# Kernel tuning notes

Measured on AMD Instinct MI355X. Metric: run time of the kernel, lower is better.

Reference implementation:

```python
import jax, jax.numpy as jnp
import numpy as np

N_VERTS = 5000
N_FACES = 10000
BATCH = 2
N_PTS = 8192
OUTER_LOOP = 4
INNER_LOOP = 50
SOLVE_SCALE = 10.0
ADAM_LR = 0.01
B1, B2, EPS = 0.9, 0.999, 1e-8


def _normalize(x, eps=1e-12):
    # torch.nn.functional.normalize(p=2, dim=-1)
    n = jnp.linalg.norm(x, axis=-1, keepdims=True)
    return x / jnp.maximum(n, eps)


def _interp_bary(tri, vw):
    # tri: [M,3,3] per-point triangle attributes, vw: [M,2] barycentric (u,v)
    bary = jnp.concatenate([vw, 1.0 - vw[:, :1] - vw[:, 1:2]], axis=-1)  # [M,3]
    return jnp.einsum('mij,mi->mj', tri, bary)


def _solve_delta_vwd(qV, fid, vw, mesh_V, mesh_F, mesh_N):
    # Newton-like correspondence solve via unrolled Adam (solve_delta_vwd).
    tri_idx = mesh_F[fid]          # [M,3]
    tri_V = mesh_V[tri_idx]        # [M,3,3]
    tri_N = mesh_N[tri_idx]        # [M,3,3]
    d0 = jnp.linalg.norm(_interp_bary(tri_V, vw) - qV, axis=-1)
    delta0 = jnp.concatenate([jnp.zeros_like(vw), d0[:, None]], axis=-1)  # [M,3]
    target = qV * SOLVE_SCALE

    def loss_fn(delta):
        w = vw + delta[:, :2]
        cV = _interp_bary(tri_V, w) * SOLVE_SCALE
        cN = _normalize(_interp_bary(tri_N, w)) * SOLVE_SCALE
        match = cV + cN * delta[:, 2:3]
        return jnp.mean((match - target) ** 2)  # F.mse_loss

    def step(carry, t):
        delta, m, v = carry
        g = jax.grad(loss_fn)(delta)
        m = B1 * m + (1.0 - B1) * g
        v = B2 * v + (1.0 - B2) * g * g
        mhat = m / (1.0 - B1 ** t)
        vhat = v / (1.0 - B2 ** t)
        delta = delta - ADAM_LR * mhat / (jnp.sqrt(vhat) + EPS)
        return (delta, m, v), None

    ts = jnp.arange(1, INNER_LOOP + 1, dtype=qV.dtype)
    zeros = jnp.zeros_like(delta0)
    (delta, _, _), _ = jax.lax.scan(step, (delta0, zeros, zeros), ts)
    return delta


def _forward(verts, mesh_V, mesh_N, mesh_F):
    b, n, _ = verts.shape
    # init_corres_spt: KNN (K=1) of query points against triangle centers
    centers = mesh_V[mesh_F].mean(axis=1)  # [F,3]
    d2 = ((verts ** 2).sum(-1)[..., None]
          + (centers ** 2).sum(-1)[None, None, :]
          - 2.0 * jnp.einsum('bnd,fd->bnf', verts, centers))  # [b,n,F]
    fidx = jnp.argmin(d2, axis=-1)                             # [b,n]
    fid = fidx.reshape(-1)
    qV = verts.reshape(-1, 3)
    vw = jnp.full((b * n, 2), 1.0 / 3.0, dtype=verts.dtype)
    # update_corres_spt (method='uvd'): outer triwalk loop.
    # triwalk is an external CPU mesh-walker; we use the module's documented
    # fallback when triwalk is None: vw <- vw + delta (face index unchanged).
    for _ in range(OUTER_LOOP):
        delta = _solve_delta_vwd(qV, fid, vw, mesh_V, mesh_F, mesh_N)
        vw = vw + delta[:, :2]
    outlier_mask = jnp.zeros((b, n), dtype=bool)  # max_dist = inf
    return fidx, vw.reshape(b, n, 2), outlier_mask


def setup_inputs() -> dict:
    key = jax.random.key(0)
    k1, k2, k3, k4 = jax.random.split(key, 4)
    mesh_V = jax.random.normal(k1, (N_VERTS, 3), dtype=jnp.float32)
    mesh_F = jax.random.randint(k2, (N_FACES, 3), 0, N_VERTS)
    mesh_N = _normalize(jax.random.normal(k3, (N_VERTS, 3), dtype=jnp.float32))
    verts = jax.random.normal(k4, (BATCH, N_PTS, 3), dtype=jnp.float32)
    return {"verts": verts, "mesh_V": mesh_V, "mesh_N": mesh_N, "mesh_F": mesh_F}


def reference(verts, mesh_V, mesh_N, mesh_F):
    return _forward(verts, mesh_V, mesh_N, mesh_F)
```

## Files before the change

kernel.cpp:

```cpp
#include <hip/hip_runtime.h>
#include <math.h>
#include <stdint.h>

constexpr int kVerts = 5000;
constexpr int kFaces = 10000;
constexpr int kPts   = 16384;
constexpr int kOuter = 4;
constexpr int kInner = 50;

#define SCALE 10.0f

#define KNN_WAVES 16
#define KNN_FQ    4
constexpr int kQuarter     = kFaces / KNN_FQ;
constexpr int kPtsPerLane  = 2;
constexpr int kPtsPerBlock = 64 * kPtsPerLane;
constexpr int kPtGroups    = kPts / kPtsPerBlock;

struct BiasTabP { float rb[kInner + 2][2]; };
constexpr BiasTabP make_tabp() {
    BiasTabP t{};
    float b1 = 1.0f, b2 = 1.0f;
    for (int i = 0; i < kInner; ++i) {
        b1 *= 0.9f; b2 *= 0.999f;
        t.rb[i][0] = 1.0f / (1.0f - b1);
        t.rb[i][1] = 1.0f / (1.0f - b2);
    }
    t.rb[kInner][0]     = t.rb[kInner - 1][0];
    t.rb[kInner][1]     = t.rb[kInner - 1][1];
    t.rb[kInner + 1][0] = t.rb[kInner - 1][0];
    t.rb[kInner + 1][1] = t.rb[kInner - 1][1];
    return t;
}
constexpr BiasTabP kTabP = make_tabp();

__global__ __launch_bounds__(256)
void centers_kernel(const float* __restrict__ mesh_V,
                    const int*   __restrict__ mesh_F,
                    float4*      __restrict__ cent)
{
    const int f = blockIdx.x * 256 + threadIdx.x;
    if (f >= kFaces) return;
    const int i0 = mesh_F[f * 3 + 0];
    const int i1 = mesh_F[f * 3 + 1];
    const int i2 = mesh_F[f * 3 + 2];
    const float cx = __fdiv_rn(__fadd_rn(__fadd_rn(mesh_V[i0*3+0], mesh_V[i1*3+0]), mesh_V[i2*3+0]), 3.0f);
    const float cy = __fdiv_rn(__fadd_rn(__fadd_rn(mesh_V[i0*3+1], mesh_V[i1*3+1]), mesh_V[i2*3+1]), 3.0f);
    const float cz = __fdiv_rn(__fadd_rn(__fadd_rn(mesh_V[i0*3+2], mesh_V[i1*3+2]), mesh_V[i2*3+2]), 3.0f);
    const float cc = __fadd_rn(__fadd_rn(__fmul_rn(cx, cx), __fmul_rn(cy, cy)),
                               __fmul_rn(cz, cz));
    cent[f] = make_float4(cx, cy, cz, cc);
}

__global__ __launch_bounds__(1024)
void knn_kernel(const float* __restrict__ verts,
                const float4* __restrict__ cent,
                float*        __restrict__ ws_d2,
                int*          __restrict__ ws_f)
{
    __shared__ float4 s_cent[kQuarter];
    __shared__ float  s_best [KNN_WAVES * kPtsPerBlock];
    __shared__ int    s_bestf[KNN_WAVES * kPtsPerBlock];

    const int tid  = threadIdx.x;
    const int lane = tid & 63;
    const int wv   = __builtin_amdgcn_readfirstlane(tid >> 6);
    const int pg   = blockIdx.x >> 2;
    const int fq   = blockIdx.x & 3;
    const int qbeg = fq * kQuarter;

    for (int i = tid; i < kQuarter; i += 1024)
        s_cent[i] = cent[qbeg + i];

    const int pA = pg * kPtsPerBlock + lane;
    const int pB = pA + 64;
    const float qxA = verts[pA * 3 + 0], qyA = verts[pA * 3 + 1], qzA = verts[pA * 3 + 2];
    const float qxB = verts[pB * 3 + 0], qyB = verts[pB * 3 + 1], qzB = verts[pB * 3 + 2];
    const float q2A = __fadd_rn(__fadd_rn(__fmul_rn(qxA, qxA), __fmul_rn(qyA, qyA)),
                                __fmul_rn(qzA, qzA));
    const float q2B = __fadd_rn(__fadd_rn(__fmul_rn(qxB, qxB), __fmul_rn(qyB, qyB)),
                                __fmul_rn(qzB, qzB));
    const float dqxA = __fmul_rn(2.0f, qxA), dqyA = __fmul_rn(2.0f, qyA), dqzA = __fmul_rn(2.0f, qzA);
    const float dqxB = __fmul_rn(2.0f, qxB), dqyB = __fmul_rn(2.0f, qyB), dqzB = __fmul_rn(2.0f, qzB);

    __syncthreads();

    const int fbeg = (wv * kQuarter) / KNN_WAVES;
    const int fend = ((wv + 1) * kQuarter) / KNN_WAVES;

    float bdA0 = INFINITY, bdA1 = INFINITY, bdB0 = INFINITY, bdB1 = INFINITY;
    int   bfA0 = 0x7fffffff, bfA1 = 0x7fffffff, bfB0 = 0x7fffffff, bfB1 = 0x7fffffff;

#define KNN_EVAL(FF, C, DQX, DQY, DQZ, Q2, BD, BF)                                    \
    {                                                                                 \
        const float dot2 = __fadd_rn(__fadd_rn(__fmul_rn((DQX), (C).x),               \
                                               __fmul_rn((DQY), (C).y)),              \
                                     __fmul_rn((DQZ), (C).z));                        \
        const float d2 = __fsub_rn(__fadd_rn((Q2), (C).w), dot2);                     \
        if (d2 < (BD)) { (BD) = d2; (BF) = (FF); }                                    \
    }

    int f = fbeg;
#pragma unroll 1
    for (; f + 8 <= fend; f += 8) {
        const float4 c0 = s_cent[f + 0];
        const float4 c1 = s_cent[f + 1];
        const float4 c2 = s_cent[f + 2];
        const float4 c3 = s_cent[f + 3];
        const float4 c4 = s_cent[f + 4];
        const float4 c5 = s_cent[f + 5];
        const float4 c6 = s_cent[f + 6];
        const float4 c7 = s_cent[f + 7];
        KNN_EVAL(qbeg + f + 0, c0, dqxA, dqyA, dqzA, q2A, bdA0, bfA0);
        KNN_EVAL(qbeg + f + 1, c1, dqxA, dqyA, dqzA, q2A, bdA1, bfA1);
        KNN_EVAL(qbeg + f + 2, c2, dqxA, dqyA, dqzA, q2A, bdA0, bfA0);
        KNN_EVAL(qbeg + f + 3, c3, dqxA, dqyA, dqzA, q2A, bdA1, bfA1);
        KNN_EVAL(qbeg + f + 4, c4, dqxA, dqyA, dqzA, q2A, bdA0, bfA0);
        KNN_EVAL(qbeg + f + 5, c5, dqxA, dqyA, dqzA, q2A, bdA1, bfA1);
        KNN_EVAL(qbeg + f + 6, c6, dqxA, dqyA, dqzA, q2A, bdA0, bfA0);
        KNN_EVAL(qbeg + f + 7, c7, dqxA, dqyA, dqzA, q2A, bdA1, bfA1);
        KNN_EVAL(qbeg + f + 0, c0, dqxB, dqyB, dqzB, q2B, bdB0, bfB0);
        KNN_EVAL(qbeg + f + 1, c1, dqxB, dqyB, dqzB, q2B, bdB1, bfB1);
        KNN_EVAL(qbeg + f + 2, c2, dqxB, dqyB, dqzB, q2B, bdB0, bfB0);
        KNN_EVAL(qbeg + f + 3, c3, dqxB, dqyB, dqzB, q2B, bdB1, bfB1);
        KNN_EVAL(qbeg + f + 4, c4, dqxB, dqyB, dqzB, q2B, bdB0, bfB0);
        KNN_EVAL(qbeg + f + 5, c5, dqxB, dqyB, dqzB, q2B, bdB1, bfB1);
        KNN_EVAL(qbeg + f + 6, c6, dqxB, dqyB, dqzB, q2B, bdB0, bfB0);
        KNN_EVAL(qbeg + f + 7, c7, dqxB, dqyB, dqzB, q2B, bdB1, bfB1);
    }
    for (; f < fend; ++f) {
        const float4 c0 = s_cent[f];
        KNN_EVAL(qbeg + f, c0, dqxA, dqyA, dqzA, q2A, bdA0, bfA0);
        KNN_EVAL(qbeg + f, c0, dqxB, dqyB, dqzB, q2B, bdB0, bfB0);
    }
#undef KNN_EVAL

    if (bdA1 < bdA0 || (bdA1 == bdA0 && bfA1 < bfA0)) { bdA0 = bdA1; bfA0 = bfA1; }
    if (bdB1 < bdB0 || (bdB1 == bdB0 && bfB1 < bfB0)) { bdB0 = bdB1; bfB0 = bfB1; }

    __syncthreads();

    s_best [wv * kPtsPerBlock + lane]      = bdA0;
    s_bestf[wv * kPtsPerBlock + lane]      = bfA0;
    s_best [wv * kPtsPerBlock + 64 + lane] = bdB0;
    s_bestf[wv * kPtsPerBlock + 64 + lane] = bfB0;
    __syncthreads();

    if (tid < kPtsPerBlock) {
        float best  = s_best[tid];
        int   bestf = s_bestf[tid];
#pragma unroll
        for (int w = 1; w < KNN_WAVES; ++w) {
            const float ob = s_best [w * kPtsPerBlock + tid];
            const int   of = s_bestf[w * kPtsPerBlock + tid];
            if (ob < best) { best = ob; bestf = of; }
        }
        const int p = pg * kPtsPerBlock + tid;
        ws_d2[fq * kPts + p] = best;
        ws_f [fq * kPts + p] = bestf;
    }
}

__global__ __launch_bounds__(64)
void solve_kernel(const float* __restrict__ verts,
                  const float* __restrict__ mesh_V,
                  const float* __restrict__ mesh_N,
                  const int*   __restrict__ mesh_F,
                  const float* __restrict__ ws_d2,
                  const int*   __restrict__ ws_f,
                  float*       __restrict__ out)
{
    const int p = blockIdx.x * 64 + threadIdx.x;

    float bdm = ws_d2[p];
    int   f   = ws_f[p];
#pragma unroll
    for (int q = 1; q < KNN_FQ; ++q) {
        const float d  = ws_d2[q * kPts + p];
        const int   ff = ws_f [q * kPts + p];
        if (d < bdm) { bdm = d; f = ff; }
    }
    out[p] = (float)f;

    const float qx = verts[p * 3 + 0];
    const float qy = verts[p * 3 + 1];
    const float qz = verts[p * 3 + 2];

    const int i0 = mesh_F[f * 3 + 0];
    const int i1 = mesh_F[f * 3 + 1];
    const int i2 = mesh_F[f * 3 + 2];

    const float V0x = mesh_V[i0*3+0], V0y = mesh_V[i0*3+1], V0z = mesh_V[i0*3+2];
    const float V1x = mesh_V[i1*3+0], V1y = mesh_V[i1*3+1], V1z = mesh_V[i1*3+2];
    const float V2x = mesh_V[i2*3+0], V2y = mesh_V[i2*3+1], V2z = mesh_V[i2*3+2];
    const float N0x = mesh_N[i0*3+0], N0y = mesh_N[i0*3+1], N0z = mesh_N[i0*3+2];
    const float N1x = mesh_N[i1*3+0], N1y = mesh_N[i1*3+1], N1z = mesh_N[i1*3+2];
    const float N2x = mesh_N[i2*3+0], N2y = mesh_N[i2*3+1], N2z = mesh_N[i2*3+2];

    const float E0x = V0x - V2x, E0y = V0y - V2y, E0z = V0z - V2z;
    const float E1x = V1x - V2x, E1y = V1y - V2y, E1z = V1z - V2z;
    const float F0x = N0x - N2x, F0y = N0y - N2y, F0z = N0z - N2z;
    const float F1x = N1x - N2x, F1y = N1y - N2y, F1z = N1z - N2z;

    const float tx = qx * SCALE, ty = qy * SCALE, tz = qz * SCALE;
    const float GS = 2.0f / (3.0f * 16384.0f);
    const float B1 = 0.9f,  ONE_M_B1 = 1.0f - 0.9f;
    const float B2 = 0.999f, ONE_M_B2 = 1.0f - 0.999f;

    float vwu = 1.0f / 3.0f, vwv = 1.0f / 3.0f;

#define SOLVE_STEP(RB1, RB2)                                                   \
    {                                                                          \
        const float bu = vwu + du;                                             \
        const float bv = vwv + dv;                                             \
        const float bw = (1.0f - bu) - bv;                                     \
        const float cVx = ((bu * V0x + bv * V1x) + bw * V2x) * SCALE;          \
        const float cVy = ((bu * V0y + bv * V1y) + bw * V2y) * SCALE;          \
        const float cVz = ((bu * V0z + bv * V1z) + bw * V2z) * SCALE;          \
        const float nrx = (bu * N0x + bv * N1x) + bw * N2x;                    \
        const float nry = (bu * N0y + bv * N1y) + bw * N2y;                    \
        const float nrz = (bu * N0z + bv * N1z) + bw * N2z;                    \
        const float nn  = (nrx * nrx + nry * nry) + nrz * nrz;                 \
        const float inv = __builtin_amdgcn_rsqf(nn);                           \
        const float nhx = nrx * inv, nhy = nry * inv, nhz = nrz * inv;         \
        const float cNx = nhx * SCALE, cNy = nhy * SCALE, cNz = nhz * SCALE;   \
        const float rx = (cVx + cNx * dd) - tx;                                \
        const float ry = (cVy + cNy * dd) - ty;                                \
        const float rz = (cVz + cNz * dd) - tz;                                \
        const float rv0  = (rx * E0x + ry * E0y) + rz * E0z;                   \
        const float rv1  = (rx * E1x + ry * E1y) + rz * E1z;                   \
        const float rn0  = (rx * F0x + ry * F0y) + rz * F0z;                   \
        const float rn1  = (rx * F1x + ry * F1y) + rz * F1z;                   \
        const float nf0  = (nhx * F0x + nhy * F0y) + nhz * F0z;                \
        const float nf1  = (nhx * F1x + nhy * F1y) + nhz * F1z;                \
        const float nr_r = (nhx * rx + nhy * ry) + nhz * rz;                   \
        const float gu = GS * (SCALE * rv0 + (dd * SCALE) * ((rn0 - nr_r * nf0) * inv)); \
        const float gv = GS * (SCALE * rv1 + (dd * SCALE) * ((rn1 - nr_r * nf1) * inv)); \
        const float gd = GS * (SCALE * nr_r);                                  \
        mAu = B1 * mAu + ONE_M_B1 * gu;                                        \
        mAv = B1 * mAv + ONE_M_B1 * gv;                                        \
        mAd = B1 * mAd + ONE_M_B1 * gd;                                        \
        vAu = B2 * vAu + ONE_M_B2 * (gu * gu);                                 \
        vAv = B2 * vAv + ONE_M_B2 * (gv * gv);                                 \
        vAd = B2 * vAd + ONE_M_B2 * (gd * gd);                                 \
        const float su = __builtin_amdgcn_rsqf(vAu * (RB2) + 1e-16f);          \
        const float sv = __builtin_amdgcn_rsqf(vAv * (RB2) + 1e-16f);          \
        const float sd = __builtin_amdgcn_rsqf(vAd * (RB2) + 1e-16f);          \
        du -= 0.01f * (mAu * (RB1)) * su;                                      \
        dv -= 0.01f * (mAv * (RB1)) * sv;                                      \
        dd -= 0.01f * (mAd * (RB1)) * sd;                                      \
    }

    for (int outer = 0; outer < kOuter; ++outer) {
        const float bw0 = (1.0f - vwu) - vwv;
        const float px = ((vwu * V0x + vwv * V1x) + bw0 * V2x);
        const float py = ((vwu * V0y + vwv * V1y) + bw0 * V2y);
        const float pz = ((vwu * V0z + vwv * V1z) + bw0 * V2z);
        const float dx = px - qx, dy = py - qy, dz = pz - qz;
        const float d0 = __builtin_amdgcn_sqrtf((dx * dx + dy * dy) + dz * dz);

        float du = 0.0f, dv = 0.0f, dd = d0;
        float mAu = 0.0f, mAv = 0.0f, mAd = 0.0f;
        float vAu = 0.0f, vAv = 0.0f, vAd = 0.0f;

        float rbA1 = kTabP.rb[0][0], rbA2 = kTabP.rb[0][1];
        float rbB1 = kTabP.rb[1][0], rbB2 = kTabP.rb[1][1];
#pragma unroll 1
        for (int i2 = 0; i2 < kInner / 2; ++i2) {
            const float n1a = kTabP.rb[2 * i2 + 2][0];
            const float n2a = kTabP.rb[2 * i2 + 2][1];
            const float n1b = kTabP.rb[2 * i2 + 3][0];
            const float n2b = kTabP.rb[2 * i2 + 3][1];
            SOLVE_STEP(rbA1, rbA2);
            SOLVE_STEP(rbB1, rbB2);
            rbA1 = n1a; rbA2 = n2a; rbB1 = n1b; rbB2 = n2b;
        }
        vwu += du;
        vwv += dv;
    }
#undef SOLVE_STEP

    out[kPts + 2 * p + 0] = vwu;
    out[kPts + 2 * p + 1] = vwv;
    out[3 * kPts + p]     = 0.0f;
}

extern "C" void kernel_launch(void* const* d_in, const int* in_sizes, int n_in,
                              void* d_out, int out_size, void* d_ws, size_t ws_size,
                              hipStream_t stream) {
    const float* verts  = (const float*)d_in[0];
    const float* mesh_V = (const float*)d_in[1];
    const float* mesh_N = (const float*)d_in[2];
    const int*   mesh_F = (const int*)d_in[3];
    float* out = (float*)d_out;

    float4* ws_cent = (float4*)d_ws;
    float*  ws_d2   = (float*)((char*)d_ws + kFaces * sizeof(float4));
    int*    ws_f    = (int*)((char*)ws_d2 + KNN_FQ * kPts * sizeof(float));

    hipLaunchKernelGGL(centers_kernel, dim3((kFaces + 255) / 256), dim3(256), 0, stream,
                       mesh_V, mesh_F, ws_cent);
    hipLaunchKernelGGL(knn_kernel,     dim3(kPtGroups * KNN_FQ), dim3(1024), 0, stream,
                       verts, ws_cent, ws_d2, ws_f);
    hipLaunchKernelGGL(solve_kernel,   dim3(kPts / 64), dim3(64), 0, stream,
                       verts, mesh_V, mesh_N, mesh_F, ws_d2, ws_f, out);
}
```

Before: 132.5 us.

## Split each point's Adam solve across four lanes with DPP broadcasts

The solve kernel now assigns four lanes to each query point. Lanes 0, 1 and 2 own the u, v and d components of the Adam state, and lane 3 is idle. Each step broadcasts the delta components within a quad using DPP, so every lane computes its own gradient component and Adam update. This raises thread-level parallelism: the old launch had only 256 single-wave blocks for 16384 points, which leaves most of the GPU idle. The cost is redundant per-lane evaluation of the interpolation and normal, an unused fourth lane, and a serial dependency through the cross-lane broadcasts.

```diff
diff --git a/kernel.cpp b/kernel.cpp
--- a/kernel.cpp
+++ b/kernel.cpp
@@ -161,7 +161,13 @@
     }
 }
 
-__global__ __launch_bounds__(64)
+template<int K>
+__device__ __forceinline__ float qbcast(float v) {
+    return __int_as_float(__builtin_amdgcn_update_dpp(
+        0, __float_as_int(v), K * 0x55 , 0xF, 0xF, true));
+}
+
+__global__ __launch_bounds__(256)
 void solve_kernel(const float* __restrict__ verts,
                   const float* __restrict__ mesh_V,
                   const float* __restrict__ mesh_N,
@@ -170,7 +176,11 @@
                   const int*   __restrict__ ws_f,
                   float*       __restrict__ out)
 {
-    const int p = blockIdx.x * 64 + threadIdx.x;
+    const int t  = blockIdx.x * 256 + threadIdx.x;
+    const int p  = t >> 2;
+    const int ch = t & 3;
+    const bool isV = (ch == 1);
+    const bool isD = (ch >= 2);
 
     float bdm = ws_d2[p];
     int   f   = ws_f[p];
@@ -180,7 +190,7 @@
         const int   ff = ws_f [q * kPts + p];
         if (d < bdm) { bdm = d; f = ff; }
     }
-    out[p] = (float)f;
+    if (ch == 0) out[p] = (float)f;
 
     const float qx = verts[p * 3 + 0];
     const float qy = verts[p * 3 + 1];
@@ -202,15 +212,25 @@
     const float F0x = N0x - N2x, F0y = N0y - N2y, F0z = N0z - N2z;
     const float F1x = N1x - N2x, F1y = N1y - N2y, F1z = N1z - N2z;
 
+    const float Aux = isV ? E1x : E0x;
+    const float Auy = isV ? E1y : E0y;
+    const float Auz = isV ? E1z : E0z;
+    const float Bx  = isD ? 0.0f : (isV ? F1x : F0x);
+    const float By  = isD ? 0.0f : (isV ? F1y : F0y);
+    const float Bz  = isD ? 0.0f : (isV ? F1z : F0z);
+
     const float tx = qx * SCALE, ty = qy * SCALE, tz = qz * SCALE;
     const float GS = 2.0f / (3.0f * 16384.0f);
-    const float B1 = 0.9f,  ONE_M_B1 = 1.0f - 0.9f;
-    const float B2 = 0.999f, ONE_M_B2 = 1.0f - 0.999f;
+    const float B1c = 0.9f,  ONE_M_B1 = 1.0f - 0.9f;
+    const float B2c = 0.999f, ONE_M_B2 = 1.0f - 0.999f;
 
     float vwu = 1.0f / 3.0f, vwv = 1.0f / 3.0f;
 
 #define SOLVE_STEP(RB1, RB2)                                                   \
     {                                                                          \
+        const float du = qbcast<0>(dlt);                                       \
+        const float dv = qbcast<1>(dlt);                                       \
+        const float dd = qbcast<2>(dlt);                                       \
         const float bu = vwu + du;                                             \
         const float bv = vwv + dv;                                             \
         const float bw = (1.0f - bu) - bv;                                     \
@@ -227,28 +247,18 @@
         const float rx = (cVx + cNx * dd) - tx;                                \
         const float ry = (cVy + cNy * dd) - ty;                                \
         const float rz = (cVz + cNz * dd) - tz;                                \
-        const float rv0  = (rx * E0x + ry * E0y) + rz * E0z;                   \
-        const float rv1  = (rx * E1x + ry * E1y) + rz * E1z;                   \
-        const float rn0  = (rx * F0x + ry * F0y) + rz * F0z;                   \
-        const float rn1  = (rx * F1x + ry * F1y) + rz * F1z;                   \
-        const float nf0  = (nhx * F0x + nhy * F0y) + nhz * F0z;                \
-        const float nf1  = (nhx * F1x + nhy * F1y) + nhz * F1z;                \
-        const float nr_r = (nhx * rx + nhy * ry) + nhz * rz;                   \
-        const float gu = GS * (SCALE * rv0 + (dd * SCALE) * ((rn0 - nr_r * nf0) * inv)); \
-        const float gv = GS * (SCALE * rv1 + (dd * SCALE) * ((rn1 - nr_r * nf1) * inv)); \
-        const float gd = GS * (SCALE * nr_r);                                  \
-        mAu = B1 * mAu + ONE_M_B1 * gu;                                        \
-        mAv = B1 * mAv + ONE_M_B1 * gv;                                        \
-        mAd = B1 * mAd + ONE_M_B1 * gd;                                        \
-        vAu = B2 * vAu + ONE_M_B2 * (gu * gu);                                 \
-        vAv = B2 * vAv + ONE_M_B2 * (gv * gv);                                 \
-        vAd = B2 * vAd + ONE_M_B2 * (gd * gd);                                 \
-        const float su = __builtin_amdgcn_rsqf(vAu * (RB2) + 1e-16f);          \
-        const float sv = __builtin_amdgcn_rsqf(vAv * (RB2) + 1e-16f);          \
-        const float sd = __builtin_amdgcn_rsqf(vAd * (RB2) + 1e-16f);          \
-        du -= 0.01f * (mAu * (RB1)) * su;                                      \
-        dv -= 0.01f * (mAv * (RB1)) * sv;                                      \
-        dd -= 0.01f * (mAd * (RB1)) * sd;                                      \
+        const float Ax = isD ? nhx : Aux;                                      \
+        const float Ay = isD ? nhy : Auy;                                      \
+        const float Az = isD ? nhz : Auz;                                      \
+        const float dotA = (rx * Ax + ry * Ay) + rz * Az;                      \
+        const float dotB = (rx * Bx + ry * By) + rz * Bz;                      \
+        const float nhB  = (nhx * Bx + nhy * By) + nhz * Bz;                   \
+        const float nr_r = qbcast<2>(dotA);                                    \
+        const float g = GS * (SCALE * dotA + (dd * SCALE) * ((dotB - nr_r * nhB) * inv)); \
+        mA = B1c * mA + ONE_M_B1 * g;                                          \
+        vA = B2c * vA + ONE_M_B2 * (g * g);                                    \
+        const float s = __builtin_amdgcn_rsqf(vA * (RB2) + 1e-16f);            \
+        dlt -= 0.01f * (mA * (RB1)) * s;                                       \
     }
 
     for (int outer = 0; outer < kOuter; ++outer) {
@@ -259,30 +269,31 @@
         const float dx = px - qx, dy = py - qy, dz = pz - qz;
         const float d0 = __builtin_amdgcn_sqrtf((dx * dx + dy * dy) + dz * dz);
 
-        float du = 0.0f, dv = 0.0f, dd = d0;
-        float mAu = 0.0f, mAv = 0.0f, mAd = 0.0f;
-        float vAu = 0.0f, vAv = 0.0f, vAd = 0.0f;
+        float dlt = isD ? d0 : 0.0f;
+        float mA  = 0.0f, vA = 0.0f;
 
         float rbA1 = kTabP.rb[0][0], rbA2 = kTabP.rb[0][1];
         float rbB1 = kTabP.rb[1][0], rbB2 = kTabP.rb[1][1];
 #pragma unroll 1
-        for (int i2 = 0; i2 < kInner / 2; ++i2) {
-            const float n1a = kTabP.rb[2 * i2 + 2][0];
-            const float n2a = kTabP.rb[2 * i2 + 2][1];
-            const float n1b = kTabP.rb[2 * i2 + 3][0];
-            const float n2b = kTabP.rb[2 * i2 + 3][1];
+        for (int it2 = 0; it2 < kInner / 2; ++it2) {
+            const float n1a = kTabP.rb[2 * it2 + 2][0];
+            const float n2a = kTabP.rb[2 * it2 + 2][1];
+            const float n1b = kTabP.rb[2 * it2 + 3][0];
+            const float n2b = kTabP.rb[2 * it2 + 3][1];
             SOLVE_STEP(rbA1, rbA2);
             SOLVE_STEP(rbB1, rbB2);
             rbA1 = n1a; rbA2 = n2a; rbB1 = n1b; rbB2 = n2b;
         }
-        vwu += du;
-        vwv += dv;
+        vwu += qbcast<0>(dlt);
+        vwv += qbcast<1>(dlt);
     }
 #undef SOLVE_STEP
 
-    out[kPts + 2 * p + 0] = vwu;
-    out[kPts + 2 * p + 1] = vwv;
-    out[3 * kPts + p]     = 0.0f;
+    if (ch == 0) {
+        out[kPts + 2 * p + 0] = vwu;
+        out[kPts + 2 * p + 1] = vwv;
+        out[3 * kPts + p]     = 0.0f;
+    }
 }
 
 extern "C" void kernel_launch(void* const* d_in, const int* in_sizes, int n_in,
@@ -302,6 +313,6 @@
                        mesh_V, mesh_F, ws_cent);
     hipLaunchKernelGGL(knn_kernel,     dim3(kPtGroups * KNN_FQ), dim3(1024), 0, stream,
                        verts, ws_cent, ws_d2, ws_f);
-    hipLaunchKernelGGL(solve_kernel,   dim3(kPts / 64), dim3(64), 0, stream,
+    hipLaunchKernelGGL(solve_kernel,   dim3(kPts * 4 / 256), dim3(256), 0, stream,
                        verts, mesh_V, mesh_N, mesh_F, ws_d2, ws_f, out);
 }
```

Measured after the change: 122.8 us. -7.3%, faster.
